# Optimization experiments

Hardware: AMD Instinct MI355X
Metric: run time of the kernel (lower is better)

Reference implementation:

```python
import jax, jax.numpy as jnp
import numpy as np

B, T, IN, OUT = 32, 1024, 1024, 1024
DT = 1.0
TAU_MIN, TAU_MAX = 5.0, 25.0


def setup_inputs() -> dict:
    key = jax.random.key(0)
    k1, k2, k3 = jax.random.split(key, 3)
    bound = 1.0 / np.sqrt(IN)
    inputs = jax.random.normal(k1, (B, T, IN), dtype=jnp.float32)
    weight = jax.random.uniform(k2, (OUT, IN), dtype=jnp.float32, minval=-bound, maxval=bound)
    bias = jnp.zeros((OUT,), dtype=jnp.float32)
    # per-neuron decay alpha = exp(-dt/tau), tau ~ U[tau_min, tau_max]
    tau = jax.random.uniform(k3, (OUT,), dtype=jnp.float32, minval=TAU_MIN, maxval=TAU_MAX)
    decay = jnp.exp(-DT / tau)
    return {"inputs": inputs, "weight": weight, "bias": bias, "decay": decay}


def reference(inputs, weight, bias, decay):
    # time-distributed linear projection: [B,T,IN] @ [OUT,IN]^T -> [B,T,OUT]
    current = jnp.einsum('bti,oi->bto', inputs, weight) + bias
    u0 = jnp.zeros((inputs.shape[0], weight.shape[0]), dtype=current.dtype)

    def step(u, x_t):
        # leaky integrator: u_t = alpha*u_{t-1} + (1-alpha)*x_t
        u = decay * u + (1.0 - decay) * x_t
        return u, u

    # scan over time: move T to leading axis
    _, u_seq = jax.lax.scan(step, u0, jnp.swapaxes(current, 0, 1))
    return jnp.swapaxes(u_seq, 0, 1)  # [B,T,OUT]
```

## Files before the change

kernel.cpp:

```cpp
#include <hip/hip_runtime.h>

#define M_DIM 32768
#define N_DIM 1024
#define K_DIM 1024
#define T_DIM 1024
#define B_DIM 32
#define NCHUNK 8
#define CHUNK_T 128

typedef unsigned int uint32;
typedef __attribute__((ext_vector_type(8))) short short8;
typedef __attribute__((ext_vector_type(8))) unsigned short ushort8v;
typedef __attribute__((ext_vector_type(4))) float floatx4;

__device__ __forceinline__ unsigned short f2bf(float f) {
    uint32 u = __float_as_uint(f);
    uint32 r = u + 0x7fffu + ((u >> 16) & 1u);
    return (unsigned short)(r >> 16);
}

__device__ __forceinline__ void async_load16(const void* g, void* s) {
    __builtin_amdgcn_global_load_lds(
        (const __attribute__((address_space(1))) void*)g,
        (__attribute__((address_space(3))) void*)s,
        16, 0, 0);
}

__device__ __forceinline__ short8 pk8(floatx4 a, floatx4 b) {
    union { short8 s; uint32 d[4]; } u;
    asm("v_cvt_pk_bf16_f32 %0, %1, %2" : "=v"(u.d[0]) : "v"(a[0]), "v"(a[1]));
    asm("v_cvt_pk_bf16_f32 %0, %1, %2" : "=v"(u.d[1]) : "v"(a[2]), "v"(a[3]));
    asm("v_cvt_pk_bf16_f32 %0, %1, %2" : "=v"(u.d[2]) : "v"(b[0]), "v"(b[1]));
    asm("v_cvt_pk_bf16_f32 %0, %1, %2" : "=v"(u.d[3]) : "v"(b[2]), "v"(b[3]));
    return u.s;
}

#define FENCE  asm volatile("" ::: "memory")
#define BAR    __builtin_amdgcn_s_barrier()
#define LGKM0  asm volatile("s_waitcnt lgkmcnt(0)" ::: "memory")
#define SCHED0 __builtin_amdgcn_sched_barrier(0)
#define VMW(N) asm volatile("s_waitcnt vmcnt(" #N ")" ::: "memory")

#define STAGE_B(JH, T, PB) do {                                              \
        size_t kof_ = (size_t)(T) * 64 + sc8;                                \
        _Pragma("unroll") for (int q_ = 0; q_ < 2; ++q_) {                   \
            int br_ = (q_ * 2 + (tid >> 8)) * 64 + (JH) * 32 + (t3 & 31);    \
            int dr_ = (q_ * 2 + (wid >> 2)) * 64 + (JH) * 32 + (wid & 3) * 8;\
            async_load16(Bw + (size_t)(bn0 + br_) * K_DIM + kof_,            \
                         smem + (PB) * 32768 + 16384 + dr_ * 64);            \
        } } while (0)

#define LD_A8(IH) do {                                                       \
        const unsigned short* As_ = smem + pb * 32768;                       \
        _Pragma("unroll") for (int ii = 0; ii < 4; ++ii) {                   \
            int r_ = wm * 128 + (IH) * 64 + ii * 16 + l15;                   \
            _Pragma("unroll") for (int ks = 0; ks < 2; ++ks) {               \
                int c_ = ks * 4 + quad;                                      \
                af[ii][ks] = *(const short8*)&As_[r_ * 64 +                  \
                                                 ((c_ ^ (l15 & 7)) * 8)];    \
            } } } while (0)
#define LD_B8(JH) do {                                                       \
        const unsigned short* Bs_ = smem + pb * 32768 + 16384;               \
        _Pragma("unroll") for (int jj = 0; jj < 2; ++jj) {                   \
            int r_ = wn * 64 + ((JH) * 2 + jj) * 16 + l15;                   \
            _Pragma("unroll") for (int ks = 0; ks < 2; ++ks) {               \
                int c_ = ks * 4 + quad;                                      \
                bfr[(JH) * 2 + jj][ks] = *(const short8*)&Bs_[r_ * 64 +      \
                                                 ((c_ ^ (l15 & 7)) * 8)];    \
            } } } while (0)
#define MM8(IH, JH) do {                                                     \
        __builtin_amdgcn_s_setprio(1);                                       \
        _Pragma("unroll") for (int ii = 0; ii < 4; ++ii)                     \
        _Pragma("unroll") for (int jj = 0; jj < 2; ++jj)                     \
        _Pragma("unroll") for (int ks = 0; ks < 2; ++ks)                     \
            acc[(IH) * 4 + ii][(JH) * 2 + jj] =                              \
                __builtin_amdgcn_mfma_f32_16x16x32_bf16(                     \
                    af[ii][ks], bfr[(JH) * 2 + jj][ks],                      \
                    acc[(IH) * 4 + ii][(JH) * 2 + jj], 0, 0, 0);             \
        __builtin_amdgcn_s_setprio(0);                                       \
    } while (0)

#define AISSUE(P, T) do {                                                    \
        const float* p_ = abase[P] + (T) * 64;                               \
        asm volatile("global_load_dwordx4 %0, %1, off"                       \
                     : "=&v"(ar[2 * (P)]) : "v"(p_));                        \
        asm volatile("global_load_dwordx4 %0, %1, off offset:16"             \
                     : "=&v"(ar[2 * (P) + 1]) : "v"(p_));                    \
    } while (0)
#define AWRITE(P, PBDST) do {                                                \
        int row_ = (P) * 64 + (tid >> 3);                                    \
        int cs_  = (tid & 7) ^ (row_ & 7);                                   \
        *(short8*)&smem[(PBDST) * 32768 + row_ * 64 + cs_ * 8] =             \
            pk8(ar[2 * (P)], ar[2 * (P) + 1]);                               \
    } while (0)

__global__ void cast_f32_bf16_x8(const float* __restrict__ src,
                                 unsigned short* __restrict__ dst, int n8) {
    int i = blockIdx.x * blockDim.x + threadIdx.x;
    if (i < n8) {
        const float4* s4 = (const float4*)src;
        float4 v0 = s4[(size_t)i * 2];
        float4 v1 = s4[(size_t)i * 2 + 1];
        ushort8v o;
        o[0] = f2bf(v0.x); o[1] = f2bf(v0.y); o[2] = f2bf(v0.z); o[3] = f2bf(v0.w);
        o[4] = f2bf(v1.x); o[5] = f2bf(v1.y); o[6] = f2bf(v1.z); o[7] = f2bf(v1.w);
        ((ushort8v*)dst)[i] = o;
    }
}

__global__ __launch_bounds__(512, 2) void gemm_fused(
    const float* __restrict__ X32,
    const unsigned short* __restrict__ Bw,
    const float* __restrict__ bias,
    unsigned short* __restrict__ outBf) {
    extern __shared__ __align__(16) unsigned short smem[];

    const int tid  = threadIdx.x;
    const int lane = tid & 63;
    const int wid  = tid >> 6;
    const int l15  = lane & 15;
    const int quad = lane >> 4;
    const int wm   = wid >> 2;
    const int wn   = wid & 3;

    const int L   = blockIdx.y * gridDim.x + blockIdx.x;
    const int xcd = L & 7;
    const int s   = L >> 3;
    const int bn0 = (s & 3) * 256;
    const int bm0 = (xcd * 16 + (s >> 2)) * 256;

    const int t3  = tid >> 3;
    const int sc8 = ((tid & 7) ^ (t3 & 7)) * 8;

    const float* abase[4];
#pragma unroll
    for (int p = 0; p < 4; ++p)
        abase[p] = X32 + (size_t)(bm0 + p * 64 + (tid >> 3)) * K_DIM + (tid & 7) * 8;

    floatx4 acc[8][4];
#pragma unroll
    for (int i = 0; i < 8; ++i)
#pragma unroll
        for (int j = 0; j < 4; ++j)
            acc[i][j] = (floatx4){0.f, 0.f, 0.f, 0.f};

    short8 af[4][2];
    short8 bfr[4][2];
    floatx4 ar[8];

    AISSUE(0, 0); AISSUE(1, 0); AISSUE(2, 0); AISSUE(3, 0);
    STAGE_B(0, 0, 0); STAGE_B(1, 0, 0);
    VMW(2); SCHED0;
    AWRITE(0, 0); AWRITE(1, 0); AWRITE(2, 0); AWRITE(3, 0);
    AISSUE(0, 1); STAGE_B(0, 1, 1); AISSUE(1, 1); AISSUE(2, 1);
    STAGE_B(1, 1, 1); AISSUE(3, 1);
    VMW(10); LGKM0; FENCE; BAR;

#define TILE_MAIN(G) do {                                                    \
        const int pb = (G) & 1;                                              \
        LD_A8(0); LD_B8(0);                                                  \
        VMW(8); SCHED0; AWRITE(0, pb ^ 1); AISSUE(0, (G) + 2);               \
        LGKM0; BAR; SCHED0; MM8(0, 0); BAR;                                  \
        LD_B8(1); STAGE_B(0, (G) + 2, pb);                                   \
        VMW(8); SCHED0; AWRITE(1, pb ^ 1); AISSUE(1, (G) + 2);               \
        LGKM0; BAR; SCHED0; MM8(0, 1); BAR;                                  \
        LD_A8(1);                                                            \
        VMW(8); SCHED0; AWRITE(2, pb ^ 1); AISSUE(2, (G) + 2);               \
        LGKM0; BAR; SCHED0; MM8(1, 0); BAR;                                  \
        STAGE_B(1, (G) + 2, pb);                                             \
        VMW(8); SCHED0; AWRITE(3, pb ^ 1); AISSUE(3, (G) + 2);               \
        LGKM0; BAR; SCHED0; MM8(1, 1); BAR;                                  \
    } while (0)

    for (int g = 0; g < 14; ++g) TILE_MAIN(g);

    {
        const int pb = 0;
        LD_A8(0); LD_B8(0);
        VMW(8); SCHED0; AWRITE(0, 1);
        LGKM0; BAR; SCHED0; MM8(0, 0); BAR;
        LD_B8(1);
        VMW(5); SCHED0; AWRITE(1, 1);
        LGKM0; BAR; SCHED0; MM8(0, 1); BAR;
        LD_A8(1);
        VMW(3); SCHED0; AWRITE(2, 1);
        LGKM0; BAR; SCHED0; MM8(1, 0); BAR;
        VMW(0); SCHED0; AWRITE(3, 1);
        LGKM0; BAR; SCHED0; MM8(1, 1); BAR;
    }
    {
        const int pb = 1;
        LD_A8(0); LD_B8(0); LGKM0; BAR; SCHED0; MM8(0, 0); BAR;
        LD_B8(1);           LGKM0; BAR; SCHED0; MM8(0, 1); BAR;
        LD_A8(1);           LGKM0; BAR; SCHED0; MM8(1, 0); BAR;
                            LGKM0; BAR; SCHED0; MM8(1, 1); BAR;
    }
#undef TILE_MAIN

    float bb[4];
#pragma unroll
    for (int j = 0; j < 4; ++j) bb[j] = bias[bn0 + wn * 64 + j * 16 + l15];
#pragma unroll
    for (int i = 0; i < 8; ++i) {
        int rowb = bm0 + wm * 128 + i * 16 + quad * 4;
#pragma unroll
        for (int r = 0; r < 4; ++r) {
            size_t rb = (size_t)(rowb + r) * N_DIM + bn0 + wn * 64 + l15;
#pragma unroll
            for (int j = 0; j < 4; ++j)
                outBf[rb + j * 16] = f2bf(acc[i][j][r] + bb[j]);
        }
    }
}

__global__ __launch_bounds__(512, 2) void gemm_8phase(
    const unsigned short* __restrict__ A,
    const unsigned short* __restrict__ Bw,
    const float* __restrict__ bias,
    unsigned short* __restrict__ outBf) {
    extern __shared__ __align__(16) unsigned short smem[];

    const int tid  = threadIdx.x;
    const int lane = tid & 63;
    const int wid  = tid >> 6;
    const int l15  = lane & 15;
    const int quad = lane >> 4;
    const int wm   = wid >> 2;
    const int wn   = wid & 3;

    const int L   = blockIdx.y * gridDim.x + blockIdx.x;
    const int xcd = L & 7;
    const int s   = L >> 3;
    const int bn0 = (s & 3) * 256;
    const int bm0 = (xcd * 16 + (s >> 2)) * 256;

    const int t3  = tid >> 3;
    const int sc8 = ((tid & 7) ^ (t3 & 7)) * 8;

#define STAGE_A(IH, T, PB) do {                                              \
        size_t kof_ = (size_t)(T) * 64 + sc8;                                \
        _Pragma("unroll") for (int q_ = 0; q_ < 2; ++q_) {                   \
            int ar_ = q_ * 128 + (IH) * 64 + t3;                             \
            int dr_ = q_ * 128 + (IH) * 64 + wid * 8;                        \
            async_load16(A + (size_t)(bm0 + ar_) * K_DIM + kof_,             \
                         smem + (PB) * 32768 + dr_ * 64);                    \
        } } while (0)

    floatx4 acc[8][4];
#pragma unroll
    for (int i = 0; i < 8; ++i)
#pragma unroll
        for (int j = 0; j < 4; ++j)
            acc[i][j] = (floatx4){0.f, 0.f, 0.f, 0.f};

    short8 af[4][2];
    short8 bfr[4][2];

    const int NT = K_DIM / 64;

    STAGE_A(0, 0, 0); STAGE_A(1, 0, 0); STAGE_B(0, 0, 0); STAGE_B(1, 0, 0);
    STAGE_A(0, 1, 1); STAGE_B(1, 1, 1); STAGE_B(0, 1, 1);
    asm volatile("s_waitcnt vmcnt(6)" ::: "memory");
    FENCE; BAR;

    for (int g = 0; g < NT; ++g) {
        const int pb = g & 1;
        const int po = pb ^ 1;

        LD_A8(0); LD_B8(0);
        if (g + 1 < NT) STAGE_A(1, g + 1, po);
        FENCE; BAR; LGKM0; SCHED0;
        MM8(0, 0);
        SCHED0; FENCE; BAR;

        LD_B8(1);
        if (g + 2 < NT) STAGE_A(0, g + 2, pb);
        FENCE; BAR; LGKM0; SCHED0;
        MM8(0, 1);
        SCHED0; FENCE; BAR;

        LD_A8(1);
        if (g + 2 < NT) STAGE_B(1, g + 2, pb);
        FENCE; BAR; LGKM0; SCHED0;
        MM8(1, 0);
        SCHED0; FENCE; BAR;

        if (g + 2 < NT) STAGE_B(0, g + 2, pb);
        if (g < NT - 2) {
            asm volatile("s_waitcnt vmcnt(6)" ::: "memory");
        } else if (g == NT - 2) {
            asm volatile("s_waitcnt vmcnt(0)" ::: "memory");
        }
        FENCE; BAR; LGKM0; SCHED0;
        MM8(1, 1);
        SCHED0; FENCE; BAR;
    }
    asm volatile("s_waitcnt vmcnt(0)" ::: "memory");

    float bb[4];
#pragma unroll
    for (int j = 0; j < 4; ++j) bb[j] = bias[bn0 + wn * 64 + j * 16 + l15];
#pragma unroll
    for (int i = 0; i < 8; ++i) {
        int rowb = bm0 + wm * 128 + i * 16 + quad * 4;
#pragma unroll
        for (int r = 0; r < 4; ++r) {
            size_t rb = (size_t)(rowb + r) * N_DIM + bn0 + wn * 64 + l15;
#pragma unroll
            for (int j = 0; j < 4; ++j)
                outBf[rb + j * 16] = f2bf(acc[i][j][r] + bb[j]);
        }
    }
#undef STAGE_A
}

__global__ __launch_bounds__(256) void scan_carry2(
    const uint32* __restrict__ cur32,
    const float* __restrict__ decay,
    float* __restrict__ carry) {
    int tid   = blockIdx.x * 256 + threadIdx.x;
    int o2    = tid & 511;
    int chunk = (tid >> 9) & (NCHUNK - 1);
    int b     = tid >> 12;
    int o     = o2 * 2;
    size_t base = ((size_t)b * T_DIM + (size_t)chunk * CHUNK_T) * (N_DIM / 2) + o2;
    float2 a2 = *(const float2*)&decay[o];
    float a0 = a2.x, a1 = a2.y;
    float c0 = 1.f - a0, c1 = 1.f - a1;
    float u0 = 0.f, u1 = 0.f;
    for (int t0 = 0; t0 < CHUNK_T; t0 += 32) {
        uint32 x[32];
#pragma unroll
        for (int k = 0; k < 32; ++k)
            x[k] = cur32[base + (size_t)(t0 + k) * (N_DIM / 2)];
#pragma unroll
        for (int k = 0; k < 32; ++k) {
            float lo = __uint_as_float(x[k] << 16);
            float hi = __uint_as_float(x[k] & 0xffff0000u);
            u0 = a0 * u0 + c0 * lo;
            u1 = a1 * u1 + c1 * hi;
        }
    }
    float2* cw = (float2*)&carry[((size_t)b * NCHUNK + chunk) * N_DIM + o];
    *cw = (float2){u0, u1};
}

__global__ __launch_bounds__(256) void scan_apply2(
    const uint32* __restrict__ cur32,
    const float* __restrict__ decay,
    const float* __restrict__ carry,
    float* __restrict__ out) {
    int tid   = blockIdx.x * 256 + threadIdx.x;
    int o2    = tid & 511;
    int chunk = (tid >> 9) & (NCHUNK - 1);
    int b     = tid >> 12;
    int o     = o2 * 2;
    size_t base = ((size_t)b * T_DIM + (size_t)chunk * CHUNK_T) * (N_DIM / 2) + o2;
    float2 a2 = *(const float2*)&decay[o];
    float a0 = a2.x, a1 = a2.y;
    float c0 = 1.f - a0, c1 = 1.f - a1;

    float A0 = a0, A1 = a1;
#pragma unroll
    for (int i = 0; i < 7; ++i) { A0 *= A0; A1 *= A1; }

    float u0 = 0.f, u1 = 0.f;
    const float* cb = carry + (size_t)b * NCHUNK * N_DIM + o;
    for (int i = 0; i < chunk; ++i) {
        float2 cv = *(const float2*)&cb[(size_t)i * N_DIM];
        u0 = cv.x + A0 * u0;
        u1 = cv.y + A1 * u1;
    }

    float2* out2 = (float2*)out;
    size_t obase = ((size_t)b * T_DIM + (size_t)chunk * CHUNK_T) * (N_DIM / 2) + o2;
    for (int t0 = 0; t0 < CHUNK_T; t0 += 32) {
        uint32 x[32];
#pragma unroll
        for (int k = 0; k < 32; ++k)
            x[k] = cur32[base + (size_t)(t0 + k) * (N_DIM / 2)];
#pragma unroll
        for (int k = 0; k < 32; ++k) {
            float lo = __uint_as_float(x[k] << 16);
            float hi = __uint_as_float(x[k] & 0xffff0000u);
            u0 = a0 * u0 + c0 * lo;
            u1 = a1 * u1 + c1 * hi;
            out2[obase + (size_t)(t0 + k) * (N_DIM / 2)] = (float2){u0, u1};
        }
    }
}

__global__ void scan_f32_inplace(float* __restrict__ buf,
                                 const float* __restrict__ decay) {
    int tid = blockIdx.x * 64 + threadIdx.x;
    int o = tid & (N_DIM - 1);
    size_t base = ((size_t)(tid >> 10) << 20) + o;
    float a = decay[o];
    float c = 1.f - a;
    float u = 0.f;
    for (int t0 = 0; t0 < 1024; t0 += 16) {
        float x[16];
#pragma unroll
        for (int k = 0; k < 16; ++k)
            x[k] = buf[base + (size_t)(t0 + k) * N_DIM];
#pragma unroll
        for (int k = 0; k < 16; ++k) {
            u = a * u + c * x[k];
            buf[base + (size_t)(t0 + k) * N_DIM] = u;
        }
    }
}

__global__ __launch_bounds__(256) void gemm_mfma(
    const unsigned short* __restrict__ A,
    const unsigned short* __restrict__ Bw,
    const float* __restrict__ bias,
    unsigned short* outBf,
    float* outF) {
    __shared__ unsigned short As[128 * 64];
    __shared__ unsigned short Bs[128 * 64];

    const int tid  = threadIdx.x;
    const int lane = tid & 63;
    const int wid  = tid >> 6;
    const int l15  = lane & 15;
    const int quad = lane >> 4;
    const int wm   = wid >> 1;
    const int wn   = wid & 1;

    const int L    = blockIdx.y * gridDim.x + blockIdx.x;
    const int xcd  = L & 7;
    const int s    = L >> 3;
    const int bn0  = (s & 7) * 128;
    const int bm0  = (xcd * 32 + (s >> 3)) * 128;

    floatx4 acc[4][4];
#pragma unroll
    for (int i = 0; i < 4; ++i)
#pragma unroll
        for (int j = 0; j < 4; ++j)
            acc[i][j] = (floatx4){0.f, 0.f, 0.f, 0.f};

    for (int kt = 0; kt < K_DIM / 64; ++kt) {
        const int k0 = kt * 64;
#pragma unroll
        for (int q = 0; q < 4; ++q) {
            int slot = q * 256 + tid;
            int row  = slot >> 3;
            int chq  = slot & 7;
            int scq  = chq ^ (row & 7);
            async_load16(A + (size_t)(bm0 + row) * K_DIM + k0 + scq * 8,
                         &As[(q * 256 + wid * 64) * 8]);
        }
#pragma unroll
        for (int q = 0; q < 4; ++q) {
            int slot = q * 256 + tid;
            int row  = slot >> 3;
            int chq  = slot & 7;
            int scq  = chq ^ (row & 7);
            async_load16(Bw + (size_t)(bn0 + row) * K_DIM + k0 + scq * 8,
                         &Bs[(q * 256 + wid * 64) * 8]);
        }
        __syncthreads();

#pragma unroll
        for (int ks = 0; ks < 2; ++ks) {
            short8 af[4], bfr[4];
#pragma unroll
            for (int i = 0; i < 4; ++i) {
                int r = wm * 64 + i * 16 + l15;
                int c = ks * 4 + quad;
                af[i] = *(const short8*)&As[r * 64 + ((c ^ (r & 7)) * 8)];
            }
#pragma unroll
            for (int j = 0; j < 4; ++j) {
                int r = wn * 64 + j * 16 + l15;
                int c = ks * 4 + quad;
                bfr[j] = *(const short8*)&Bs[r * 64 + ((c ^ (r & 7)) * 8)];
            }
#pragma unroll
            for (int i = 0; i < 4; ++i)
#pragma unroll
                for (int j = 0; j < 4; ++j)
                    acc[i][j] = __builtin_amdgcn_mfma_f32_16x16x32_bf16(
                        af[i], bfr[j], acc[i][j], 0, 0, 0);
        }
        __syncthreads();
    }

#pragma unroll
    for (int j = 0; j < 4; ++j) {
        int col = bn0 + wn * 64 + j * 16 + l15;
        float bb = bias[col];
#pragma unroll
        for (int i = 0; i < 4; ++i) {
            int rowb = bm0 + wm * 64 + i * 16 + quad * 4;
#pragma unroll
            for (int r = 0; r < 4; ++r) {
                float v = acc[i][j][r] + bb;
                size_t idx = (size_t)(rowb + r) * N_DIM + col;
                if (outBf) outBf[idx] = f2bf(v);
                else       outF[idx]  = v;
            }
        }
    }
}

__global__ void gemm_naive(const float* __restrict__ X, const float* __restrict__ W,
                           const float* __restrict__ bias, float* __restrict__ out) {
    __shared__ float As[16][17], Bs[16][17];
    int tx = threadIdx.x, ty = threadIdx.y;
    int m0 = blockIdx.y * 16, n0 = blockIdx.x * 16;
    float acc = 0.f;
    for (int k0 = 0; k0 < K_DIM; k0 += 16) {
        As[ty][tx] = X[(size_t)(m0 + ty) * K_DIM + k0 + tx];
        Bs[ty][tx] = W[(size_t)(n0 + ty) * K_DIM + k0 + tx];
        __syncthreads();
#pragma unroll
        for (int kk = 0; kk < 16; ++kk) acc += As[ty][kk] * Bs[tx][kk];
        __syncthreads();
    }
    out[(size_t)(m0 + ty) * N_DIM + n0 + tx] = acc + bias[n0 + tx];
}

extern "C" void kernel_launch(void* const* d_in, const int* in_sizes, int n_in,
                              void* d_out, int out_size, void* d_ws, size_t ws_size,
                              hipStream_t stream) {
    const float* X     = (const float*)d_in[0];
    const float* Wt    = (const float*)d_in[1];
    const float* bias  = (const float*)d_in[2];
    const float* decay = (const float*)d_in[3];
    float* out = (float*)d_out;

    static bool fused_ok = [] {
        return hipFuncSetAttribute(reinterpret_cast<const void*>(gemm_fused),
                                   hipFuncAttributeMaxDynamicSharedMemorySize,
                                   131072) == hipSuccess;
    }();
    static bool lds128_ok = [] {
        return hipFuncSetAttribute(reinterpret_cast<const void*>(gemm_8phase),
                                   hipFuncAttributeMaxDynamicSharedMemorySize,
                                   131072) == hipSuccess;
    }();

    const size_t A_bytes  = (size_t)M_DIM * K_DIM * 2;
    const size_t W_bytes  = (size_t)N_DIM * K_DIM * 2;
    const size_t C_bytes  = (size_t)M_DIM * N_DIM * 2;
    const size_t cr_bytes = (size_t)B_DIM * NCHUNK * N_DIM * 4;
    const size_t need_new  = W_bytes + C_bytes + cr_bytes;
    const size_t need_mid  = A_bytes + W_bytes;
    const size_t need_full = A_bytes + W_bytes + C_bytes + cr_bytes;
    const int scan_threads = B_DIM * NCHUNK * N_DIM / 2;

    if (fused_ok && ws_size >= need_new) {
        unsigned short* Wbf = (unsigned short*)d_ws;
        unsigned short* Cbf = (unsigned short*)((char*)d_ws + W_bytes);
        float* carry = (float*)((char*)d_ws + W_bytes + C_bytes);
        cast_f32_bf16_x8<<<(N_DIM * K_DIM / 8 + 255) / 256, 256, 0, stream>>>(Wt, Wbf, N_DIM * K_DIM / 8);
        gemm_fused<<<dim3(4, 128), 512, 131072, stream>>>(X, Wbf, bias, Cbf);
        scan_carry2<<<scan_threads / 256, 256, 0, stream>>>((const uint32*)Cbf, decay, carry);
        scan_apply2<<<scan_threads / 256, 256, 0, stream>>>((const uint32*)Cbf, decay, carry, out);
    } else if (lds128_ok && ws_size >= need_full) {
        unsigned short* Abf = (unsigned short*)d_ws;
        unsigned short* Wbf = (unsigned short*)((char*)d_ws + A_bytes);
        unsigned short* Cbf = (unsigned short*)((char*)d_ws + A_bytes + W_bytes);
        float* carry = (float*)((char*)d_ws + A_bytes + W_bytes + C_bytes);
        cast_f32_bf16_x8<<<(M_DIM * K_DIM / 8 + 255) / 256, 256, 0, stream>>>(X, Abf, M_DIM * K_DIM / 8);
        cast_f32_bf16_x8<<<(N_DIM * K_DIM / 8 + 255) / 256, 256, 0, stream>>>(Wt, Wbf, N_DIM * K_DIM / 8);
        gemm_8phase<<<dim3(4, 128), 512, 131072, stream>>>(Abf, Wbf, bias, Cbf);
        scan_carry2<<<scan_threads / 256, 256, 0, stream>>>((const uint32*)Cbf, decay, carry);
        scan_apply2<<<scan_threads / 256, 256, 0, stream>>>((const uint32*)Cbf, decay, carry, out);
    } else if (ws_size >= need_mid) {
        unsigned short* Abf = (unsigned short*)d_ws;
        unsigned short* Wbf = (unsigned short*)((char*)d_ws + A_bytes);
        cast_f32_bf16_x8<<<(M_DIM * K_DIM / 8 + 255) / 256, 256, 0, stream>>>(X, Abf, M_DIM * K_DIM / 8);
        cast_f32_bf16_x8<<<(N_DIM * K_DIM / 8 + 255) / 256, 256, 0, stream>>>(Wt, Wbf, N_DIM * K_DIM / 8);
        gemm_mfma<<<dim3(N_DIM / 128, M_DIM / 128), 256, 0, stream>>>(Abf, Wbf, bias, nullptr, out);
        scan_f32_inplace<<<512, 64, 0, stream>>>(out, decay);
    } else {
        gemm_naive<<<dim3(N_DIM / 16, M_DIM / 16), dim3(16, 16), 0, stream>>>(X, Wt, bias, out);
        scan_f32_inplace<<<512, 64, 0, stream>>>(out, decay);
    }
}
```

Measured before the change: 153.8 us.

## Fuse chunk carry computation into GEMM epilogue and reorder pipeline barriers

The separate scan_carry2 kernel is removed. Each GEMM wave now computes, in its epilogue, the decay-weighted sum of its 128-row (one time chunk) accumulator tile per output column using powers of decay and cross-lane shuffles, then writes the chunk carry directly. This saves one kernel launch and a full re-read of the bf16 current tensor. The main loop's wait/barrier order is also rearranged so the LDS writes for the next stage happen after the MFMA block rather than before it. The carry is now computed from fp32 accumulators instead of bf16-rounded values, which changes numerics slightly, and the extra epilogue math adds register pressure.

New measurement: 133.0 us, median of 2. 13.5% less time.

```diff
diff --git a/kernel.cpp b/kernel.cpp
--- a/kernel.cpp
+++ b/kernel.cpp
@@ -108,11 +108,13 @@
     }
 }
 
-__global__ __launch_bounds__(512, 2) void gemm_fused(
+__global__ __launch_bounds__(512, 2) void gemm_fused2(
     const float* __restrict__ X32,
     const unsigned short* __restrict__ Bw,
     const float* __restrict__ bias,
-    unsigned short* __restrict__ outBf) {
+    const float* __restrict__ decay,
+    unsigned short* __restrict__ outBf,
+    float* __restrict__ carry) {
     extern __shared__ __align__(16) unsigned short smem[];
 
     const int tid  = threadIdx.x;
@@ -150,52 +152,62 @@
 
     AISSUE(0, 0); AISSUE(1, 0); AISSUE(2, 0); AISSUE(3, 0);
     STAGE_B(0, 0, 0); STAGE_B(1, 0, 0);
-    VMW(2); SCHED0;
+    VMW(4); SCHED0;
     AWRITE(0, 0); AWRITE(1, 0); AWRITE(2, 0); AWRITE(3, 0);
     AISSUE(0, 1); STAGE_B(0, 1, 1); AISSUE(1, 1); AISSUE(2, 1);
     STAGE_B(1, 1, 1); AISSUE(3, 1);
-    VMW(10); LGKM0; FENCE; BAR;
+    LGKM0; VMW(12); FENCE; BAR;
 
 #define TILE_MAIN(G) do {                                                    \
         const int pb = (G) & 1;                                              \
+        const int po = pb ^ 1;                                               \
         LD_A8(0); LD_B8(0);                                                  \
-        VMW(8); SCHED0; AWRITE(0, pb ^ 1); AISSUE(0, (G) + 2);               \
-        LGKM0; BAR; SCHED0; MM8(0, 0); BAR;                                  \
-        LD_B8(1); STAGE_B(0, (G) + 2, pb);                                   \
-        VMW(8); SCHED0; AWRITE(1, pb ^ 1); AISSUE(1, (G) + 2);               \
-        LGKM0; BAR; SCHED0; MM8(0, 1); BAR;                                  \
+        VMW(10); FENCE; BAR; LGKM0; SCHED0;                                  \
+        MM8(0, 0);                                                           \
+        SCHED0; AWRITE(0, po); AISSUE(0, (G) + 2); FENCE; BAR;               \
+        LD_B8(1);                                                            \
+        VMW(8); FENCE; BAR; LGKM0; SCHED0;                                   \
+        MM8(0, 1);                                                           \
+        SCHED0; AWRITE(1, po); STAGE_B(0, (G) + 2, pb); AISSUE(1, (G) + 2);  \
+        FENCE; BAR;                                                          \
         LD_A8(1);                                                            \
-        VMW(8); SCHED0; AWRITE(2, pb ^ 1); AISSUE(2, (G) + 2);               \
-        LGKM0; BAR; SCHED0; MM8(1, 0); BAR;                                  \
-        STAGE_B(1, (G) + 2, pb);                                             \
-        VMW(8); SCHED0; AWRITE(3, pb ^ 1); AISSUE(3, (G) + 2);               \
-        LGKM0; BAR; SCHED0; MM8(1, 1); BAR;                                  \
+        VMW(10); FENCE; BAR; LGKM0; SCHED0;                                  \
+        MM8(1, 0);                                                           \
+        SCHED0; AWRITE(2, po); AISSUE(2, (G) + 2); FENCE; BAR;               \
+        VMW(8); FENCE; BAR; LGKM0; SCHED0;                                   \
+        MM8(1, 1);                                                           \
+        SCHED0; AWRITE(3, po); STAGE_B(1, (G) + 2, pb); AISSUE(3, (G) + 2);  \
+        FENCE; BAR;                                                          \
     } while (0)
 
     for (int g = 0; g < 14; ++g) TILE_MAIN(g);
+#undef TILE_MAIN
 
     {
         const int pb = 0;
         LD_A8(0); LD_B8(0);
-        VMW(8); SCHED0; AWRITE(0, 1);
-        LGKM0; BAR; SCHED0; MM8(0, 0); BAR;
+        VMW(10); FENCE; BAR; LGKM0; SCHED0;
+        MM8(0, 0);
+        SCHED0; AWRITE(0, 1); FENCE; BAR;
         LD_B8(1);
-        VMW(5); SCHED0; AWRITE(1, 1);
-        LGKM0; BAR; SCHED0; MM8(0, 1); BAR;
+        VMW(6); FENCE; BAR; LGKM0; SCHED0;
+        MM8(0, 1);
+        SCHED0; AWRITE(1, 1); FENCE; BAR;
         LD_A8(1);
-        VMW(3); SCHED0; AWRITE(2, 1);
-        LGKM0; BAR; SCHED0; MM8(1, 0); BAR;
-        VMW(0); SCHED0; AWRITE(3, 1);
-        LGKM0; BAR; SCHED0; MM8(1, 1); BAR;
+        VMW(4); FENCE; BAR; LGKM0; SCHED0;
+        MM8(1, 0);
+        SCHED0; AWRITE(2, 1); FENCE; BAR;
+        VMW(0); FENCE; BAR; LGKM0; SCHED0;
+        MM8(1, 1);
+        SCHED0; AWRITE(3, 1); FENCE; BAR;
     }
     {
         const int pb = 1;
-        LD_A8(0); LD_B8(0); LGKM0; BAR; SCHED0; MM8(0, 0); BAR;
-        LD_B8(1);           LGKM0; BAR; SCHED0; MM8(0, 1); BAR;
-        LD_A8(1);           LGKM0; BAR; SCHED0; MM8(1, 0); BAR;
-                            LGKM0; BAR; SCHED0; MM8(1, 1); BAR;
-    }
-#undef TILE_MAIN
+        LD_A8(0); LD_B8(0); FENCE; BAR; LGKM0; SCHED0; MM8(0, 0); SCHED0; FENCE; BAR;
+        LD_B8(1);           FENCE; BAR; LGKM0; SCHED0; MM8(0, 1); SCHED0; FENCE; BAR;
+        LD_A8(1);           FENCE; BAR; LGKM0; SCHED0; MM8(1, 0); SCHED0; FENCE; BAR;
+                            FENCE; BAR; LGKM0; SCHED0; MM8(1, 1); SCHED0; FENCE; BAR;
+    }
 
     float bb[4];
 #pragma unroll
@@ -209,6 +221,37 @@
 #pragma unroll
             for (int j = 0; j < 4; ++j)
                 outBf[rb + j * 16] = f2bf(acc[i][j][r] + bb[j]);
+        }
+    }
+
+    {
+        const int q4 = quad * 4;
+        const int bchk = ((bm0 >> 10) * NCHUNK) + ((bm0 >> 7) & 7) + wm;
+        float* cdst = carry + (size_t)bchk * N_DIM + bn0 + wn * 64;
+#pragma unroll
+        for (int j = 0; j < 4; ++j) {
+            float a  = decay[bn0 + wn * 64 + j * 16 + l15];
+            float a2 = a * a, a4 = a2 * a2, a8 = a4 * a4, a16 = a8 * a8;
+            float S = 0.f;
+#pragma unroll
+            for (int r = 0; r < 4; ++r) {
+                int n = 15 - q4 - r;
+                float w = 1.f;
+                w *= (n & 1) ? a  : 1.f;
+                w *= (n & 2) ? a2 : 1.f;
+                w *= (n & 4) ? a4 : 1.f;
+                w *= (n & 8) ? a8 : 1.f;
+#pragma unroll
+                for (int ii = 0; ii < 8; ++ii) {
+                    S = fmaf(w, acc[7 - ii][j][r], S);
+                    w *= a16;
+                }
+            }
+            S += __shfl_xor(S, 16, 64);
+            S += __shfl_xor(S, 32, 64);
+            float a32 = a16 * a16, a64 = a32 * a32, a128 = a64 * a64;
+            float cv = (1.f - a) * S + bb[j] * (1.f - a128);
+            if (quad == 0) cdst[j * 16 + l15] = cv;
         }
     }
 }
@@ -217,7 +260,9 @@
     const unsigned short* __restrict__ A,
     const unsigned short* __restrict__ Bw,
     const float* __restrict__ bias,
-    unsigned short* __restrict__ outBf) {
+    const float* __restrict__ decay,
+    unsigned short* __restrict__ outBf,
+    float* __restrict__ carry) {
     extern __shared__ __align__(16) unsigned short smem[];
 
     const int tid  = threadIdx.x;
@@ -311,38 +356,38 @@
                 outBf[rb + j * 16] = f2bf(acc[i][j][r] + bb[j]);
         }
     }
+
+    {
+        const int q4 = quad * 4;
+        const int bchk = ((bm0 >> 10) * NCHUNK) + ((bm0 >> 7) & 7) + wm;
+        float* cdst = carry + (size_t)bchk * N_DIM + bn0 + wn * 64;
+#pragma unroll
+        for (int j = 0; j < 4; ++j) {
+            float a  = decay[bn0 + wn * 64 + j * 16 + l15];
+            float a2 = a * a, a4 = a2 * a2, a8 = a4 * a4, a16 = a8 * a8;
+            float S = 0.f;
+#pragma unroll
+            for (int r = 0; r < 4; ++r) {
+                int n = 15 - q4 - r;
+                float w = 1.f;
+                w *= (n & 1) ? a  : 1.f;
+                w *= (n & 2) ? a2 : 1.f;
+                w *= (n & 4) ? a4 : 1.f;
+                w *= (n & 8) ? a8 : 1.f;
+#pragma unroll
+                for (int ii = 0; ii < 8; ++ii) {
+                    S = fmaf(w, acc[7 - ii][j][r], S);
+                    w *= a16;
+                }
+            }
+            S += __shfl_xor(S, 16, 64);
+            S += __shfl_xor(S, 32, 64);
+            float a32 = a16 * a16, a64 = a32 * a32, a128 = a64 * a64;
+            float cv = (1.f - a) * S + bb[j] * (1.f - a128);
+            if (quad == 0) cdst[j * 16 + l15] = cv;
+        }
+    }
 #undef STAGE_A
-}
-
-__global__ __launch_bounds__(256) void scan_carry2(
-    const uint32* __restrict__ cur32,
-    const float* __restrict__ decay,
-    float* __restrict__ carry) {
-    int tid   = blockIdx.x * 256 + threadIdx.x;
-    int o2    = tid & 511;
-    int chunk = (tid >> 9) & (NCHUNK - 1);
-    int b     = tid >> 12;
-    int o     = o2 * 2;
-    size_t base = ((size_t)b * T_DIM + (size_t)chunk * CHUNK_T) * (N_DIM / 2) + o2;
-    float2 a2 = *(const float2*)&decay[o];
-    float a0 = a2.x, a1 = a2.y;
-    float c0 = 1.f - a0, c1 = 1.f - a1;
-    float u0 = 0.f, u1 = 0.f;
-    for (int t0 = 0; t0 < CHUNK_T; t0 += 32) {
-        uint32 x[32];
-#pragma unroll
-        for (int k = 0; k < 32; ++k)
-            x[k] = cur32[base + (size_t)(t0 + k) * (N_DIM / 2)];
-#pragma unroll
-        for (int k = 0; k < 32; ++k) {
-            float lo = __uint_as_float(x[k] << 16);
-            float hi = __uint_as_float(x[k] & 0xffff0000u);
-            u0 = a0 * u0 + c0 * lo;
-            u1 = a1 * u1 + c1 * hi;
-        }
-    }
-    float2* cw = (float2*)&carry[((size_t)b * NCHUNK + chunk) * N_DIM + o];
-    *cw = (float2){u0, u1};
 }
 
 __global__ __launch_bounds__(256) void scan_apply2(
@@ -533,7 +578,7 @@
     float* out = (float*)d_out;
 
     static bool fused_ok = [] {
-        return hipFuncSetAttribute(reinterpret_cast<const void*>(gemm_fused),
+        return hipFuncSetAttribute(reinterpret_cast<const void*>(gemm_fused2),
                                    hipFuncAttributeMaxDynamicSharedMemorySize,
                                    131072) == hipSuccess;
     }();
@@ -557,8 +602,7 @@
         unsigned short* Cbf = (unsigned short*)((char*)d_ws + W_bytes);
         float* carry = (float*)((char*)d_ws + W_bytes + C_bytes);
         cast_f32_bf16_x8<<<(N_DIM * K_DIM / 8 + 255) / 256, 256, 0, stream>>>(Wt, Wbf, N_DIM * K_DIM / 8);
-        gemm_fused<<<dim3(4, 128), 512, 131072, stream>>>(X, Wbf, bias, Cbf);
-        scan_carry2<<<scan_threads / 256, 256, 0, stream>>>((const uint32*)Cbf, decay, carry);
+        gemm_fused2<<<dim3(4, 128), 512, 131072, stream>>>(X, Wbf, bias, decay, Cbf, carry);
         scan_apply2<<<scan_threads / 256, 256, 0, stream>>>((const uint32*)Cbf, decay, carry, out);
     } else if (lds128_ok && ws_size >= need_full) {
         unsigned short* Abf = (unsigned short*)d_ws;
@@ -567,8 +611,7 @@
         float* carry = (float*)((char*)d_ws + A_bytes + W_bytes + C_bytes);
         cast_f32_bf16_x8<<<(M_DIM * K_DIM / 8 + 255) / 256, 256, 0, stream>>>(X, Abf, M_DIM * K_DIM / 8);
         cast_f32_bf16_x8<<<(N_DIM * K_DIM / 8 + 255) / 256, 256, 0, stream>>>(Wt, Wbf, N_DIM * K_DIM / 8);
-        gemm_8phase<<<dim3(4, 128), 512, 131072, stream>>>(Abf, Wbf, bias, Cbf);
-        scan_carry2<<<scan_threads / 256, 256, 0, stream>>>((const uint32*)Cbf, decay, carry);
+        gemm_8phase<<<dim3(4, 128), 512, 131072, stream>>>(Abf, Wbf, bias, decay, Cbf, carry);
         scan_apply2<<<scan_threads / 256, 256, 0, stream>>>((const uint32*)Cbf, decay, carry, out);
     } else if (ws_size >= need_mid) {
         unsigned short* Abf = (unsigned short*)d_ws;
```
